# Kernel optimization log

Hardware: AMD Instinct MI355X
Metric: run time of the kernel (lower is better)

The kernel has to match this reference:

```python
import jax, jax.numpy as jnp
import numpy as np

THRESHOLD = 0.5
NEG_POS_RATIO = 3
ALPHA = 1.0
BETA = 1.0
IGNORE_INDEX = 255

B, P, C, O = 16, 16384, 21, 16
H = W = 256


def cxcy_to_xy(c):
    return jnp.concatenate([c[..., :2] - c[..., 2:] / 2, c[..., :2] + c[..., 2:] / 2], axis=-1)


def xy_to_cxcy(xy):
    return jnp.concatenate([(xy[..., :2] + xy[..., 2:]) / 2, xy[..., 2:] - xy[..., :2]], axis=-1)


def cxcy_to_gcxgcy(cxcy, priors_cxcy):
    return jnp.concatenate([
        (cxcy[..., :2] - priors_cxcy[..., :2]) / (priors_cxcy[..., 2:] / 10.0),
        jnp.log(cxcy[..., 2:] / priors_cxcy[..., 2:]) * 5.0,
    ], axis=-1)


def jaccard(set1, set2):
    # set1 [O,4] xy, set2 [P,4] xy -> IoU [O,P]
    lo = jnp.maximum(set1[:, None, :2], set2[None, :, :2])
    hi = jnp.minimum(set1[:, None, 2:], set2[None, :, 2:])
    wh = jnp.clip(hi - lo, 0.0)
    inter = wh[..., 0] * wh[..., 1]
    a1 = (set1[:, 2] - set1[:, 0]) * (set1[:, 3] - set1[:, 1])
    a2 = (set2[:, 2] - set2[:, 0]) * (set2[:, 3] - set2[:, 1])
    return inter / (a1[:, None] + a2[None, :] - inter)


def setup_inputs() -> dict:
    key = jax.random.key(0)
    ks = jax.random.split(key, 8)
    predicted_locs = jax.random.normal(ks[0], (B, P, 4), dtype=jnp.float32)
    predicted_scores = jax.random.normal(ks[1], (B, P, C), dtype=jnp.float32)
    predicted_masks = jax.random.normal(ks[2], (B, C, H, W), dtype=jnp.float32)
    x1y1 = jax.random.uniform(ks[3], (B, O, 2), dtype=jnp.float32) * 0.8
    wh = jax.random.uniform(ks[4], (B, O, 2), dtype=jnp.float32) * 0.19 + 0.01
    boxes = jnp.concatenate([x1y1, x1y1 + wh], axis=-1)  # valid xy boxes
    pc = jax.random.uniform(ks[5], (P, 2), dtype=jnp.float32) * 0.9 + 0.05
    pwh = jax.random.uniform(ks[6], (P, 2), dtype=jnp.float32) * 0.28 + 0.02
    priors_cxcy = jnp.concatenate([pc, pwh], axis=-1)
    labels = jax.random.randint(ks[7], (B, O), 1, C)  # object labels, never background
    masks = jax.random.randint(jax.random.fold_in(key, 99), (B, 1, H, W), 0, C)
    return {
        'predicted_locs': predicted_locs,
        'predicted_scores': predicted_scores,
        'predicted_masks': predicted_masks,
        'boxes': boxes,
        'priors_cxcy': priors_cxcy,
        'labels': labels,
        'masks': masks,
    }


def _assign(bx, lb, priors_cxcy, priors_xy):
    # bx [O,4] xy, lb [O] int -> true_locs [P,4], true_classes [P]
    ov = jaccard(bx, priors_xy)  # [O,P]
    overlap_for_each_prior = ov.max(axis=0)       # [P]
    object_for_each_prior = ov.argmax(axis=0)     # [P]
    prior_for_each_object = ov.argmax(axis=1)     # [O]
    # guarantee every object is matched to its best prior
    object_for_each_prior = object_for_each_prior.at[prior_for_each_object].set(jnp.arange(O))
    overlap_for_each_prior = overlap_for_each_prior.at[prior_for_each_object].set(1.0)
    label_for_each_prior = lb[object_for_each_prior]
    label_for_each_prior = jnp.where(overlap_for_each_prior < THRESHOLD, 0, label_for_each_prior)
    true_locs = cxcy_to_gcxgcy(xy_to_cxcy(bx[object_for_each_prior]), priors_cxcy)
    return true_locs, label_for_each_prior


def reference(predicted_locs, predicted_scores, predicted_masks, boxes, priors_cxcy, labels, masks):
    priors_xy = cxcy_to_xy(priors_cxcy)
    true_locs, true_classes = jax.vmap(_assign, in_axes=(0, 0, None, None))(
        boxes, labels, priors_cxcy, priors_xy)  # [B,P,4], [B,P]

    pos = true_classes != 0                      # [B,P]
    pos_f = pos.astype(predicted_locs.dtype)
    n_pos = pos.sum(axis=1)                      # [B]

    # localization: L1Loss (mean over positive prior elements)
    diff = jnp.abs(predicted_locs - true_locs)
    loc_loss = (diff * pos_f[..., None]).sum() / jnp.maximum(pos_f.sum() * 4.0, 1.0)

    # confidence: CE per prior + hard negative mining
    logp = jax.nn.log_softmax(predicted_scores, axis=-1)            # [B,P,C]
    ce = -jnp.take_along_axis(logp, true_classes[..., None], axis=-1)[..., 0]  # [B,P]
    ce_pos_sum = (ce * pos_f).sum()
    ce_neg = jnp.where(pos, 0.0, ce)
    ce_neg_sorted = -jnp.sort(-ce_neg, axis=1)                      # descending
    ranks = jnp.arange(P)[None, :]
    hard = (ranks < (NEG_POS_RATIO * n_pos)[:, None]).astype(ce.dtype)
    ce_hardneg_sum = (ce_neg_sorted * hard).sum()
    conf_loss = (ce_hardneg_sum + ce_pos_sum) / n_pos.sum().astype(ce.dtype)

    # mask loss: cross_entropy2d, sum reduction then / (H*W) / B
    tgt = masks[:, 0]                                                # [B,H,W]
    valid = (tgt != IGNORE_INDEX)
    t = jnp.where(valid, tgt, 0)
    logp_m = jax.nn.log_softmax(predicted_masks, axis=1)             # [B,C,H,W]
    ce_m = -jnp.take_along_axis(logp_m, t[:, None], axis=1)[:, 0]    # [B,H,W]
    mask_loss = (ce_m * valid.astype(ce_m.dtype)).sum() / (H * W) / B

    return conf_loss + ALPHA * loc_loss + BETA * mask_loss
```

## Files before the change

kernel.cpp:

```cpp
#include <hip/hip_runtime.h>
#include <cstdint>
#include <cstddef>

#define Bn 16
#define Pn 16384
#define Cn 21
#define On 16
#define HWn 65536
#define THRESH 0.5f


__device__ __forceinline__ float waveReduceSum(float v) {
  for (int off = 32; off > 0; off >>= 1) v += __shfl_down(v, off, 64);
  return v;
}
__device__ __forceinline__ int waveReduceSumI(int v) {
  for (int off = 32; off > 0; off >>= 1) v += __shfl_down(v, off, 64);
  return v;
}

__global__ __launch_bounds__(256, 2) void k_p1mask(
    const float* __restrict__ boxes, const float* __restrict__ priors,
    const float* __restrict__ pm, const int* __restrict__ msk,
    unsigned long long* __restrict__ partials, float* __restrict__ accum) {
  const int lane = threadIdx.x & 63, wave = threadIdx.x >> 6;
  __shared__ float4 sbox[On];
  __shared__ float sarea[On];
  __shared__ unsigned long long skey[On];
  __shared__ float sr1[4];

  if (blockIdx.x >= 1024) {
    const int idx4 = (blockIdx.x - 1024) * 256 + threadIdx.x;
    const int b = idx4 >> 14;
    const int pix = (idx4 & 16383) << 2;
    int4 t4 = ((const int4*)msk)[idx4];
    const float* base = pm + (size_t)b * ((size_t)Cn * HWn) + pix;
#define M_LD(i) float4 v##i = *(const float4*)(base + (size_t)(i) * HWn);
    M_LD(0) M_LD(1) M_LD(2) M_LD(3) M_LD(4) M_LD(5) M_LD(6) M_LD(7) M_LD(8)
    M_LD(9) M_LD(10) M_LD(11) M_LD(12) M_LD(13) M_LD(14) M_LD(15) M_LD(16)
    M_LD(17) M_LD(18) M_LD(19) M_LD(20)
#undef M_LD
    asm volatile("" ::"v"(v0.x), "v"(v1.x), "v"(v2.x), "v"(v3.x), "v"(v4.x),
                 "v"(v5.x), "v"(v6.x), "v"(v7.x), "v"(v8.x), "v"(v9.x),
                 "v"(v10.x), "v"(v11.x), "v"(v12.x), "v"(v13.x), "v"(v14.x),
                 "v"(v15.x), "v"(v16.x), "v"(v17.x), "v"(v18.x), "v"(v19.x),
                 "v"(v20.x));
    __builtin_amdgcn_sched_barrier(0);
    const bool q0 = (t4.x != 255), q1 = (t4.y != 255), q2 = (t4.z != 255),
               q3 = (t4.w != 255);
    const int c0 = q0 ? t4.x : 0, c1 = q1 ? t4.y : 0, c2 = q2 ? t4.z : 0,
              c3 = q3 ? t4.w : 0;
    float s0 = 0.f, s1 = 0.f, s2 = 0.f, s3 = 0.f;
    float x0 = 0.f, x1 = 0.f, x2 = 0.f, x3 = 0.f;
#define M_ACC(i)                                                            \
  {                                                                         \
    s0 += __expf(v##i.x); s1 += __expf(v##i.y);                             \
    s2 += __expf(v##i.z); s3 += __expf(v##i.w);                             \
    if (c0 == i) x0 = v##i.x; if (c1 == i) x1 = v##i.y;                     \
    if (c2 == i) x2 = v##i.z; if (c3 == i) x3 = v##i.w;                     \
  }
    M_ACC(0) M_ACC(1) M_ACC(2) M_ACC(3) M_ACC(4) M_ACC(5) M_ACC(6) M_ACC(7)
    M_ACC(8) M_ACC(9) M_ACC(10) M_ACC(11) M_ACC(12) M_ACC(13) M_ACC(14)
    M_ACC(15) M_ACC(16) M_ACC(17) M_ACC(18) M_ACC(19) M_ACC(20)
#undef M_ACC
    float contrib = (q0 ? (__logf(s0) - x0) : 0.f) +
                    (q1 ? (__logf(s1) - x1) : 0.f) +
                    (q2 ? (__logf(s2) - x2) : 0.f) +
                    (q3 ? (__logf(s3) - x3) : 0.f);
    float r = waveReduceSum(contrib);
    if (lane == 0) sr1[wave] = r;
    __syncthreads();
    if (threadIdx.x == 0)
      atomicAdd(&accum[3], sr1[0] + sr1[1] + sr1[2] + sr1[3]);
    return;
  }

  const int b = blockIdx.x >> 6;
  const int p0 = (blockIdx.x & 63) << 8;
  const int p = p0 + threadIdx.x;
  if (threadIdx.x < On) {
    float4 bx = ((const float4*)boxes)[b * On + threadIdx.x];
    sbox[threadIdx.x] = bx;
    sarea[threadIdx.x] = (bx.z - bx.x) * (bx.w - bx.y);
    skey[threadIdx.x] = 0ULL;
  }
  __syncthreads();
  float4 pr = ((const float4*)priors)[p];
  const float px1 = pr.x - 0.5f * pr.z, py1 = pr.y - 0.5f * pr.w;
  const float px2 = pr.x + 0.5f * pr.z, py2 = pr.y + 0.5f * pr.w;
  const float parea = pr.z * pr.w;
#pragma unroll
  for (int o = 0; o < On; ++o) {
    float4 bx = sbox[o];
    float ix = fmaxf(fminf(px2, bx.z) - fmaxf(px1, bx.x), 0.f);
    float iy = fmaxf(fminf(py2, bx.w) - fmaxf(py1, bx.y), 0.f);
    float inter = ix * iy;
    float iou = inter / (sarea[o] + parea - inter);
    float m = iou;
#pragma unroll
    for (int off = 32; off > 0; off >>= 1) m = fmaxf(m, __shfl_xor(m, off, 64));
    unsigned long long tie = __ballot(iou == m);
    if (lane == 0) {
      int lmin = __ffsll(tie) - 1;
      unsigned minp = (unsigned)(p0 + (wave << 6) + lmin);
      unsigned long long key = ((unsigned long long)__float_as_uint(m) << 32) |
                               (unsigned long long)(0xFFFFFFFFu - minp);
      atomicMax(&skey[o], key);
    }
  }
  __syncthreads();
  if (threadIdx.x < On)
    partials[(size_t)blockIdx.x * On + threadIdx.x] = skey[threadIdx.x];
}

__global__ __launch_bounds__(256, 2) void k_assign(
    const float* __restrict__ plocs, const float* __restrict__ pscores,
    const float* __restrict__ boxes, const float* __restrict__ priors,
    const int* __restrict__ labels, const unsigned long long* __restrict__ partials,
    float* __restrict__ ce_neg, float* __restrict__ accum,
    int* __restrict__ n_pos, int* __restrict__ n_pos_total) {
  __shared__ float ssc[256 * Cn];
  __shared__ float4 sbox[On];
  __shared__ float sarea[On];
  __shared__ int slab[On];
  __shared__ int spfo[On];
  __shared__ unsigned long long skey[On];
  __shared__ float sr1[4], sr2[4];
  __shared__ int sri[4];
  const int lane = threadIdx.x & 63, wave = threadIdx.x >> 6;
  const int b = blockIdx.x >> 6;
  const int p0 = (blockIdx.x & 63) << 8;
  const int p = p0 + threadIdx.x;
  {
    const float4* src = (const float4*)(pscores + ((size_t)b * Pn + p0) * Cn);
    float4* dst = (float4*)ssc;
#pragma unroll
    for (int i = threadIdx.x; i < (256 * Cn) / 4; i += 256) dst[i] = src[i];
  }
  if (threadIdx.x < On) skey[threadIdx.x] = 0ULL;
  if (threadIdx.x < On) {
    float4 bx = ((const float4*)boxes)[b * On + threadIdx.x];
    sbox[threadIdx.x] = bx;
    sarea[threadIdx.x] = (bx.z - bx.x) * (bx.w - bx.y);
    slab[threadIdx.x] = labels[b * On + threadIdx.x];
  }
  __syncthreads();
  {
    const int o = threadIdx.x & 15, j = threadIdx.x >> 4;
    const unsigned long long* pp = partials + ((size_t)b * 64) * On;
    unsigned long long k = 0ULL;
#pragma unroll
    for (int t = 0; t < 4; ++t) {
      unsigned long long v = pp[(size_t)(j * 4 + t) * On + o];
      k = v > k ? v : k;
    }
    atomicMax(&skey[o], k);
  }
  __syncthreads();
  if (threadIdx.x < On)
    spfo[threadIdx.x] = (int)(0xFFFFFFFFu - (unsigned)(skey[threadIdx.x] & 0xFFFFFFFFULL));
  __syncthreads();

  float4 pr = ((const float4*)priors)[p];
  const float px1 = pr.x - 0.5f * pr.z, py1 = pr.y - 0.5f * pr.w;
  const float px2 = pr.x + 0.5f * pr.z, py2 = pr.y + 0.5f * pr.w;
  const float parea = pr.z * pr.w;
  float best = -1.f;
  int bobj = 0;
#pragma unroll
  for (int o = 0; o < On; ++o) {
    float4 bx = sbox[o];
    float ix = fmaxf(fminf(px2, bx.z) - fmaxf(px1, bx.x), 0.f);
    float iy = fmaxf(fminf(py2, bx.w) - fmaxf(py1, bx.y), 0.f);
    float inter = ix * iy;
    float iou = inter / (sarea[o] + parea - inter);
    if (iou > best) { best = iou; bobj = o; }
  }
#pragma unroll
  for (int o = 0; o < On; ++o) {
    if (spfo[o] == p) { bobj = o; best = 1.0f; }
  }
  const int lbl = (best < THRESH) ? 0 : slab[bobj];
  const bool pos = (lbl != 0);
  float locp = 0.f;
  if (pos) {
    float4 bx = sbox[bobj];
    float cx = 0.5f * (bx.x + bx.z), cy = 0.5f * (bx.y + bx.w);
    float w = bx.z - bx.x, h = bx.w - bx.y;
    float g0 = (cx - pr.x) / (pr.z * 0.1f);
    float g1 = (cy - pr.y) / (pr.w * 0.1f);
    float g2 = logf(w / pr.z) * 5.f;
    float g3 = logf(h / pr.w) * 5.f;
    float4 pl = ((const float4*)plocs)[b * Pn + p];
    locp = fabsf(pl.x - g0) + fabsf(pl.y - g1) + fabsf(pl.z - g2) + fabsf(pl.w - g3);
  }
  const float* my = ssc + threadIdx.x * Cn;
  float s = 0.f, xt = 0.f;
#pragma unroll
  for (int c = 0; c < Cn; ++c) {
    float v = my[c];
    s += __expf(v);
    if (c == lbl) xt = v;
  }
  float ce = __logf(s) - xt;
  ce_neg[b * Pn + p] = pos ? 0.f : ce;
  float cep = pos ? ce : 0.f;

  float r1 = waveReduceSum(locp);
  float r2 = waveReduceSum(cep);
  int ri = waveReduceSumI(pos ? 1 : 0);
  if (lane == 0) { sr1[wave] = r1; sr2[wave] = r2; sri[wave] = ri; }
  __syncthreads();
  if (threadIdx.x == 0) {
    atomicAdd(&accum[0], sr1[0] + sr1[1] + sr1[2] + sr1[3]);
    atomicAdd(&accum[1], sr2[0] + sr2[1] + sr2[2] + sr2[3]);
    int ai = sri[0] + sri[1] + sri[2] + sri[3];
    atomicAdd(&n_pos[b], ai);
    atomicAdd(n_pos_total, ai);
  }
}

__global__ __launch_bounds__(1024) void k_hardneg_final(
    const float* __restrict__ ce_neg, const int* __restrict__ n_pos,
    float* __restrict__ accum, const int* __restrict__ n_pos_total,
    int* __restrict__ done_cnt, float* __restrict__ out) {
  const int b = blockIdx.x;
  const int lane = threadIdx.x & 63, wave = threadIdx.x >> 6;
  unsigned rv[16];
#pragma unroll
  for (int i = 0; i < 16; ++i)
    rv[i] = __float_as_uint(ce_neg[b * Pn + i * 1024 + threadIdx.x]);
  int K = 3 * n_pos[b];
  if (K > Pn) K = Pn;
  __shared__ int scnt[16];
  __shared__ float ssum[16];
  unsigned lo = 0u, hi = 0x7F800000u;
  while (lo < hi) {
    unsigned mid = lo + ((hi - lo) >> 1);
    int c = 0;
#pragma unroll
    for (int i = 0; i < 16; ++i) c += (rv[i] > mid) ? 1 : 0;
    c = waveReduceSumI(c);
    if (lane == 0) scnt[wave] = c;
    __syncthreads();
    int total = 0;
#pragma unroll
    for (int w = 0; w < 16; ++w) total += scnt[w];
    if (total < K) hi = mid; else lo = mid + 1;
    __syncthreads();
  }
  const float fv = __uint_as_float(lo);
  float s = 0.f;
  int c = 0;
#pragma unroll
  for (int i = 0; i < 16; ++i) {
    if (rv[i] > lo) { s += __uint_as_float(rv[i]); c++; }
  }
  s = waveReduceSum(s);
  c = waveReduceSumI(c);
  if (lane == 0) { ssum[wave] = s; scnt[wave] = c; }
  __syncthreads();
  if (threadIdx.x == 0) {
    float tots = 0.f;
    int totc = 0;
#pragma unroll
    for (int w = 0; w < 16; ++w) { tots += ssum[w]; totc += scnt[w]; }
    atomicAdd(&accum[2], tots + (float)(K - totc) * fv);
    __threadfence();
    int prev = atomicAdd(done_cnt, 1);
    if (prev == Bn - 1) {
      float a0 = atomicAdd(&accum[0], 0.f);
      float a1 = atomicAdd(&accum[1], 0.f);
      float a2 = atomicAdd(&accum[2], 0.f);
      float a3 = atomicAdd(&accum[3], 0.f);
      float np = (float)(*n_pos_total);
      float conf = (a2 + a1) / np;
      float loc = a0 / fmaxf(np * 4.f, 1.f);
      float maskl = a3 / (float)HWn / (float)Bn;
      out[0] = conf + loc + maskl;
    }
  }
}

extern "C" void kernel_launch(void* const* d_in, const int* in_sizes, int n_in,
                              void* d_out, int out_size, void* d_ws, size_t ws_size,
                              hipStream_t stream) {
  const float* plocs   = (const float*)d_in[0];
  const float* pscores = (const float*)d_in[1];
  const float* pmasks  = (const float*)d_in[2];
  const float* boxes   = (const float*)d_in[3];
  const float* priors  = (const float*)d_in[4];
  const int*   labels  = (const int*)d_in[5];
  const int*   masks   = (const int*)d_in[6];

  char* ws = (char*)d_ws;
  float* accum = (float*)ws;
  int* n_pos = (int*)(ws + 64);
  int* n_pos_total = (int*)(ws + 128);
  int* done_cnt = (int*)(ws + 132);
  unsigned long long* partials = (unsigned long long*)(ws + 4096);
  float* ce_neg = (float*)(ws + 135168);

  (void)hipMemsetAsync(ws, 0, 144, stream);
  k_p1mask<<<2048, 256, 0, stream>>>(boxes, priors, pmasks, masks, partials, accum);
  k_assign<<<1024, 256, 0, stream>>>(plocs, pscores, boxes, priors, labels,
                                     partials, ce_neg, accum, n_pos, n_pos_total);
  k_hardneg_final<<<Bn, 1024, 0, stream>>>(ce_neg, n_pos, accum, n_pos_total,
                                           done_cnt, (float*)d_out);
}
```

Before: 227.2 us.

## Fuse all stages into one cooperative persistent kernel with grid syncs

```diff
diff --git a/kernel.cpp b/kernel.cpp
--- a/kernel.cpp
+++ b/kernel.cpp
@@ -1,6 +1,9 @@
 #include <hip/hip_runtime.h>
+#include <hip/hip_cooperative_groups.h>
 #include <cstdint>
 #include <cstddef>
+
+namespace cg = cooperative_groups;
 
 #define Bn 16
 #define Pn 16384
@@ -19,18 +22,67 @@
   return v;
 }
 
-__global__ __launch_bounds__(256, 2) void k_p1mask(
-    const float* __restrict__ boxes, const float* __restrict__ priors,
-    const float* __restrict__ pm, const int* __restrict__ msk,
-    unsigned long long* __restrict__ partials, float* __restrict__ accum) {
-  const int lane = threadIdx.x & 63, wave = threadIdx.x >> 6;
+__global__ __launch_bounds__(256, 3) void k_all(
+    const float* __restrict__ plocs, const float* __restrict__ pscores,
+    const float* __restrict__ pm, const float* __restrict__ boxes,
+    const float* __restrict__ priors, const int* __restrict__ labels,
+    const int* __restrict__ msk, unsigned long long* __restrict__ partials,
+    float* __restrict__ ce_neg, float* __restrict__ mpart,
+    float* __restrict__ apart_loc, float* __restrict__ apart_ce,
+    int* __restrict__ apart_npos, float* __restrict__ bres,
+    float* __restrict__ out) {
+  __shared__ float ssc[256 * Cn];
   __shared__ float4 sbox[On];
   __shared__ float sarea[On];
+  __shared__ int slab[On];
+  __shared__ int spfo[On];
   __shared__ unsigned long long skey[On];
-  __shared__ float sr1[4];
-
-  if (blockIdx.x >= 1024) {
-    const int idx4 = (blockIdx.x - 1024) * 256 + threadIdx.x;
+  __shared__ float sr1[4], sr2[4];
+  __shared__ int sri[4];
+  const int tid = threadIdx.x;
+  const int lane = tid & 63, wave = tid >> 6;
+  cg::grid_group grid = cg::this_grid();
+
+  for (int t = blockIdx.x; t < Bn * 64; t += gridDim.x) {
+    const int b = t >> 6;
+    const int p0 = (t & 63) << 8;
+    const int p = p0 + tid;
+    if (tid < On) {
+      float4 bx = ((const float4*)boxes)[b * On + tid];
+      sbox[tid] = bx;
+      sarea[tid] = (bx.z - bx.x) * (bx.w - bx.y);
+      skey[tid] = 0ULL;
+    }
+    __syncthreads();
+    float4 pr = ((const float4*)priors)[p];
+    const float px1 = pr.x - 0.5f * pr.z, py1 = pr.y - 0.5f * pr.w;
+    const float px2 = pr.x + 0.5f * pr.z, py2 = pr.y + 0.5f * pr.w;
+    const float parea = pr.z * pr.w;
+#pragma unroll
+    for (int o = 0; o < On; ++o) {
+      float4 bx = sbox[o];
+      float ix = fmaxf(fminf(px2, bx.z) - fmaxf(px1, bx.x), 0.f);
+      float iy = fmaxf(fminf(py2, bx.w) - fmaxf(py1, bx.y), 0.f);
+      float inter = ix * iy;
+      float iou = inter / (sarea[o] + parea - inter);
+      float m = iou;
+#pragma unroll
+      for (int off = 32; off > 0; off >>= 1) m = fmaxf(m, __shfl_xor(m, off, 64));
+      unsigned long long tie = __ballot(iou == m);
+      if (lane == 0) {
+        int lmin = __ffsll(tie) - 1;
+        unsigned minp = (unsigned)(p0 + (wave << 6) + lmin);
+        unsigned long long key = ((unsigned long long)__float_as_uint(m) << 32) |
+                                 (unsigned long long)(0xFFFFFFFFu - minp);
+        atomicMax(&skey[o], key);
+      }
+    }
+    __syncthreads();
+    if (tid < On) partials[(size_t)t * On + tid] = skey[tid];
+  }
+
+  for (int t = blockIdx.x; t < 1024; t += gridDim.x) {
+    const int idx4 = t * 256 + tid;
     const int b = idx4 >> 14;
     const int pix = (idx4 & 16383) << 2;
     int4 t4 = ((const int4*)msk)[idx4];
@@ -70,210 +122,185 @@
     float r = waveReduceSum(contrib);
     if (lane == 0) sr1[wave] = r;
     __syncthreads();
-    if (threadIdx.x == 0)
-      atomicAdd(&accum[3], sr1[0] + sr1[1] + sr1[2] + sr1[3]);
-    return;
-  }
-
-  const int b = blockIdx.x >> 6;
-  const int p0 = (blockIdx.x & 63) << 8;
-  const int p = p0 + threadIdx.x;
-  if (threadIdx.x < On) {
-    float4 bx = ((const float4*)boxes)[b * On + threadIdx.x];
-    sbox[threadIdx.x] = bx;
-    sarea[threadIdx.x] = (bx.z - bx.x) * (bx.w - bx.y);
-    skey[threadIdx.x] = 0ULL;
-  }
-  __syncthreads();
-  float4 pr = ((const float4*)priors)[p];
-  const float px1 = pr.x - 0.5f * pr.z, py1 = pr.y - 0.5f * pr.w;
-  const float px2 = pr.x + 0.5f * pr.z, py2 = pr.y + 0.5f * pr.w;
-  const float parea = pr.z * pr.w;
-#pragma unroll
-  for (int o = 0; o < On; ++o) {
-    float4 bx = sbox[o];
-    float ix = fmaxf(fminf(px2, bx.z) - fmaxf(px1, bx.x), 0.f);
-    float iy = fmaxf(fminf(py2, bx.w) - fmaxf(py1, bx.y), 0.f);
-    float inter = ix * iy;
-    float iou = inter / (sarea[o] + parea - inter);
-    float m = iou;
-#pragma unroll
-    for (int off = 32; off > 0; off >>= 1) m = fmaxf(m, __shfl_xor(m, off, 64));
-    unsigned long long tie = __ballot(iou == m);
+    if (tid == 0) mpart[t] = sr1[0] + sr1[1] + sr1[2] + sr1[3];
+    __syncthreads();
+  }
+
+  __threadfence();
+  grid.sync();
+
+  for (int t = blockIdx.x; t < Bn * 64; t += gridDim.x) {
+    const int b = t >> 6;
+    const int p0 = (t & 63) << 8;
+    const int p = p0 + tid;
+    {
+      const float4* src = (const float4*)(pscores + ((size_t)b * Pn + p0) * Cn);
+      float4* dst = (float4*)ssc;
+#pragma unroll
+      for (int i = tid; i < (256 * Cn) / 4; i += 256) dst[i] = src[i];
+    }
+    if (tid < On) {
+      float4 bx = ((const float4*)boxes)[b * On + tid];
+      sbox[tid] = bx;
+      sarea[tid] = (bx.z - bx.x) * (bx.w - bx.y);
+      slab[tid] = labels[b * On + tid];
+      skey[tid] = 0ULL;
+    }
+    __syncthreads();
+    {
+      const int o = tid & 15, j = tid >> 4;
+      const unsigned long long* pp = partials + ((size_t)b * 64) * On;
+      unsigned long long k = 0ULL;
+#pragma unroll
+      for (int q = 0; q < 4; ++q) {
+        unsigned long long v = pp[(size_t)(j * 4 + q) * On + o];
+        k = v > k ? v : k;
+      }
+      atomicMax(&skey[o], k);
+    }
+    __syncthreads();
+    if (tid < On)
+      spfo[tid] = (int)(0xFFFFFFFFu - (unsigned)(skey[tid] & 0xFFFFFFFFULL));
+    __syncthreads();
+
+    float4 pr = ((const float4*)priors)[p];
+    const float px1 = pr.x - 0.5f * pr.z, py1 = pr.y - 0.5f * pr.w;
+    const float px2 = pr.x + 0.5f * pr.z, py2 = pr.y + 0.5f * pr.w;
+    const float parea = pr.z * pr.w;
+    float best = -1.f;
+    int bobj = 0;
+#pragma unroll
+    for (int o = 0; o < On; ++o) {
+      float4 bx = sbox[o];
+      float ix = fmaxf(fminf(px2, bx.z) - fmaxf(px1, bx.x), 0.f);
+      float iy = fmaxf(fminf(py2, bx.w) - fmaxf(py1, bx.y), 0.f);
+      float inter = ix * iy;
+      float iou = inter / (sarea[o] + parea - inter);
+      if (iou > best) { best = iou; bobj = o; }
+    }
+#pragma unroll
+    for (int o = 0; o < On; ++o) {
+      if (spfo[o] == p) { bobj = o; best = 1.0f; }
+    }
+    const int lbl = (best < THRESH) ? 0 : slab[bobj];
+    const bool pos = (lbl != 0);
+    float locp = 0.f;
+    if (pos) {
+      float4 bx = sbox[bobj];
+      float cx = 0.5f * (bx.x + bx.z), cy = 0.5f * (bx.y + bx.w);
+      float w = bx.z - bx.x, h = bx.w - bx.y;
+      float g0 = (cx - pr.x) / (pr.z * 0.1f);
+      float g1 = (cy - pr.y) / (pr.w * 0.1f);
+      float g2 = logf(w / pr.z) * 5.f;
+      float g3 = logf(h / pr.w) * 5.f;
+      float4 pl = ((const float4*)plocs)[b * Pn + p];
+      locp = fabsf(pl.x - g0) + fabsf(pl.y - g1) + fabsf(pl.z - g2) +
+             fabsf(pl.w - g3);
+    }
+    const float* my = ssc + tid * Cn;
+    float s = 0.f, xt = 0.f;
+#pragma unroll
+    for (int c = 0; c < Cn; ++c) {
+      float v = my[c];
+      s += __expf(v);
+      if (c == lbl) xt = v;
+    }
+    float ce = __logf(s) - xt;
+    ce_neg[b * Pn + p] = pos ? 0.f : ce;
+    float cep = pos ? ce : 0.f;
+
+    float r1 = waveReduceSum(locp);
+    float r2 = waveReduceSum(cep);
+    int ri = waveReduceSumI(pos ? 1 : 0);
+    if (lane == 0) { sr1[wave] = r1; sr2[wave] = r2; sri[wave] = ri; }
+    __syncthreads();
+    if (tid == 0) {
+      apart_loc[t] = sr1[0] + sr1[1] + sr1[2] + sr1[3];
+      apart_ce[t] = sr2[0] + sr2[1] + sr2[2] + sr2[3];
+      apart_npos[t] = sri[0] + sri[1] + sri[2] + sri[3];
+    }
+  }
+
+  __threadfence();
+  grid.sync();
+
+  if (blockIdx.x < Bn) {
+    const int b = blockIdx.x;
+    unsigned rv[64];
+#pragma unroll
+    for (int i = 0; i < 64; ++i)
+      rv[i] = __float_as_uint(ce_neg[b * Pn + i * 256 + tid]);
+    if (wave == 0) {
+      int v = apart_npos[b * 64 + lane];
+      v = waveReduceSumI(v);
+      if (lane == 0) spfo[0] = v;
+    }
+    __syncthreads();
+    int K = 3 * spfo[0];
+    if (K > Pn) K = Pn;
+    unsigned lo = 0u, hi = 0x7F800000u;
+    while (lo < hi) {
+      unsigned mid = lo + ((hi - lo) >> 1);
+      int c = 0;
+#pragma unroll
+      for (int i = 0; i < 64; ++i) c += (rv[i] > mid) ? 1 : 0;
+      c = waveReduceSumI(c);
+      if (lane == 0) sri[wave] = c;
+      __syncthreads();
+      int total = sri[0] + sri[1] + sri[2] + sri[3];
+      if (total < K) hi = mid; else lo = mid + 1;
+      __syncthreads();
+    }
+    const float fv = __uint_as_float(lo);
+    float s = 0.f;
+    int c = 0;
+#pragma unroll
+    for (int i = 0; i < 64; ++i) {
+      if (rv[i] > lo) { s += __uint_as_float(rv[i]); c++; }
+    }
+    s = waveReduceSum(s);
+    c = waveReduceSumI(c);
+    if (lane == 0) { sr1[wave] = s; sri[wave] = c; }
+    __syncthreads();
+    if (tid == 0) {
+      float tots = sr1[0] + sr1[1] + sr1[2] + sr1[3];
+      int totc = sri[0] + sri[1] + sri[2] + sri[3];
+      bres[b] = tots + (float)(K - totc) * fv;
+    }
+  }
+
+  __threadfence();
+  grid.sync();
+
+  if (blockIdx.x == 0) {
+    float l_loc = 0.f, l_ce = 0.f, l_msk = 0.f;
+    int l_np = 0;
+    for (int i = tid; i < 1024; i += 256) {
+      l_loc += apart_loc[i];
+      l_ce += apart_ce[i];
+      l_msk += mpart[i];
+      l_np += apart_npos[i];
+    }
+    float l_hn = (tid < Bn) ? bres[tid] : 0.f;
+    l_loc = waveReduceSum(l_loc);
+    l_ce = waveReduceSum(l_ce);
+    l_msk = waveReduceSum(l_msk);
+    l_hn = waveReduceSum(l_hn);
+    int l_npw = waveReduceSumI(l_np);
     if (lane == 0) {
-      int lmin = __ffsll(tie) - 1;
-      unsigned minp = (unsigned)(p0 + (wave << 6) + lmin);
-      unsigned long long key = ((unsigned long long)__float_as_uint(m) << 32) |
-                               (unsigned long long)(0xFFFFFFFFu - minp);
-      atomicMax(&skey[o], key);
-    }
-  }
-  __syncthreads();
-  if (threadIdx.x < On)
-    partials[(size_t)blockIdx.x * On + threadIdx.x] = skey[threadIdx.x];
-}
-
-__global__ __launch_bounds__(256, 2) void k_assign(
-    const float* __restrict__ plocs, const float* __restrict__ pscores,
-    const float* __restrict__ boxes, const float* __restrict__ priors,
-    const int* __restrict__ labels, const unsigned long long* __restrict__ partials,
-    float* __restrict__ ce_neg, float* __restrict__ accum,
-    int* __restrict__ n_pos, int* __restrict__ n_pos_total) {
-  __shared__ float ssc[256 * Cn];
-  __shared__ float4 sbox[On];
-  __shared__ float sarea[On];
-  __shared__ int slab[On];
-  __shared__ int spfo[On];
-  __shared__ unsigned long long skey[On];
-  __shared__ float sr1[4], sr2[4];
-  __shared__ int sri[4];
-  const int lane = threadIdx.x & 63, wave = threadIdx.x >> 6;
-  const int b = blockIdx.x >> 6;
-  const int p0 = (blockIdx.x & 63) << 8;
-  const int p = p0 + threadIdx.x;
-  {
-    const float4* src = (const float4*)(pscores + ((size_t)b * Pn + p0) * Cn);
-    float4* dst = (float4*)ssc;
-#pragma unroll
-    for (int i = threadIdx.x; i < (256 * Cn) / 4; i += 256) dst[i] = src[i];
-  }
-  if (threadIdx.x < On) skey[threadIdx.x] = 0ULL;
-  if (threadIdx.x < On) {
-    float4 bx = ((const float4*)boxes)[b * On + threadIdx.x];
-    sbox[threadIdx.x] = bx;
-    sarea[threadIdx.x] = (bx.z - bx.x) * (bx.w - bx.y);
-    slab[threadIdx.x] = labels[b * On + threadIdx.x];
-  }
-  __syncthreads();
-  {
-    const int o = threadIdx.x & 15, j = threadIdx.x >> 4;
-    const unsigned long long* pp = partials + ((size_t)b * 64) * On;
-    unsigned long long k = 0ULL;
-#pragma unroll
-    for (int t = 0; t < 4; ++t) {
-      unsigned long long v = pp[(size_t)(j * 4 + t) * On + o];
-      k = v > k ? v : k;
-    }
-    atomicMax(&skey[o], k);
-  }
-  __syncthreads();
-  if (threadIdx.x < On)
-    spfo[threadIdx.x] = (int)(0xFFFFFFFFu - (unsigned)(skey[threadIdx.x] & 0xFFFFFFFFULL));
-  __syncthreads();
-
-  float4 pr = ((const float4*)priors)[p];
-  const float px1 = pr.x - 0.5f * pr.z, py1 = pr.y - 0.5f * pr.w;
-  const float px2 = pr.x + 0.5f * pr.z, py2 = pr.y + 0.5f * pr.w;
-  const float parea = pr.z * pr.w;
-  float best = -1.f;
-  int bobj = 0;
-#pragma unroll
-  for (int o = 0; o < On; ++o) {
-    float4 bx = sbox[o];
-    float ix = fmaxf(fminf(px2, bx.z) - fmaxf(px1, bx.x), 0.f);
-    float iy = fmaxf(fminf(py2, bx.w) - fmaxf(py1, bx.y), 0.f);
-    float inter = ix * iy;
-    float iou = inter / (sarea[o] + parea - inter);
-    if (iou > best) { best = iou; bobj = o; }
-  }
-#pragma unroll
-  for (int o = 0; o < On; ++o) {
-    if (spfo[o] == p) { bobj = o; best = 1.0f; }
-  }
-  const int lbl = (best < THRESH) ? 0 : slab[bobj];
-  const bool pos = (lbl != 0);
-  float locp = 0.f;
-  if (pos) {
-    float4 bx = sbox[bobj];
-    float cx = 0.5f * (bx.x + bx.z), cy = 0.5f * (bx.y + bx.w);
-    float w = bx.z - bx.x, h = bx.w - bx.y;
-    float g0 = (cx - pr.x) / (pr.z * 0.1f);
-    float g1 = (cy - pr.y) / (pr.w * 0.1f);
-    float g2 = logf(w / pr.z) * 5.f;
-    float g3 = logf(h / pr.w) * 5.f;
-    float4 pl = ((const float4*)plocs)[b * Pn + p];
-    locp = fabsf(pl.x - g0) + fabsf(pl.y - g1) + fabsf(pl.z - g2) + fabsf(pl.w - g3);
-  }
-  const float* my = ssc + threadIdx.x * Cn;
-  float s = 0.f, xt = 0.f;
-#pragma unroll
-  for (int c = 0; c < Cn; ++c) {
-    float v = my[c];
-    s += __expf(v);
-    if (c == lbl) xt = v;
-  }
-  float ce = __logf(s) - xt;
-  ce_neg[b * Pn + p] = pos ? 0.f : ce;
-  float cep = pos ? ce : 0.f;
-
-  float r1 = waveReduceSum(locp);
-  float r2 = waveReduceSum(cep);
-  int ri = waveReduceSumI(pos ? 1 : 0);
-  if (lane == 0) { sr1[wave] = r1; sr2[wave] = r2; sri[wave] = ri; }
-  __syncthreads();
-  if (threadIdx.x == 0) {
-    atomicAdd(&accum[0], sr1[0] + sr1[1] + sr1[2] + sr1[3]);
-    atomicAdd(&accum[1], sr2[0] + sr2[1] + sr2[2] + sr2[3]);
-    int ai = sri[0] + sri[1] + sri[2] + sri[3];
-    atomicAdd(&n_pos[b], ai);
-    atomicAdd(n_pos_total, ai);
-  }
-}
-
-__global__ __launch_bounds__(1024) void k_hardneg_final(
-    const float* __restrict__ ce_neg, const int* __restrict__ n_pos,
-    float* __restrict__ accum, const int* __restrict__ n_pos_total,
-    int* __restrict__ done_cnt, float* __restrict__ out) {
-  const int b = blockIdx.x;
-  const int lane = threadIdx.x & 63, wave = threadIdx.x >> 6;
-  unsigned rv[16];
-#pragma unroll
-  for (int i = 0; i < 16; ++i)
-    rv[i] = __float_as_uint(ce_neg[b * Pn + i * 1024 + threadIdx.x]);
-  int K = 3 * n_pos[b];
-  if (K > Pn) K = Pn;
-  __shared__ int scnt[16];
-  __shared__ float ssum[16];
-  unsigned lo = 0u, hi = 0x7F800000u;
-  while (lo < hi) {
-    unsigned mid = lo + ((hi - lo) >> 1);
-    int c = 0;
-#pragma unroll
-    for (int i = 0; i < 16; ++i) c += (rv[i] > mid) ? 1 : 0;
-    c = waveReduceSumI(c);
-    if (lane == 0) scnt[wave] = c;
-    __syncthreads();
-    int total = 0;
-#pragma unroll
-    for (int w = 0; w < 16; ++w) total += scnt[w];
-    if (total < K) hi = mid; else lo = mid + 1;
-    __syncthreads();
-  }
-  const float fv = __uint_as_float(lo);
-  float s = 0.f;
-  int c = 0;
-#pragma unroll
-  for (int i = 0; i < 16; ++i) {
-    if (rv[i] > lo) { s += __uint_as_float(rv[i]); c++; }
-  }
-  s = waveReduceSum(s);
-  c = waveReduceSumI(c);
-  if (lane == 0) { ssum[wave] = s; scnt[wave] = c; }
-  __syncthreads();
-  if (threadIdx.x == 0) {
-    float tots = 0.f;
-    int totc = 0;
-#pragma unroll
-    for (int w = 0; w < 16; ++w) { tots += ssum[w]; totc += scnt[w]; }
-    atomicAdd(&accum[2], tots + (float)(K - totc) * fv);
-    __threadfence();
-    int prev = atomicAdd(done_cnt, 1);
-    if (prev == Bn - 1) {
-      float a0 = atomicAdd(&accum[0], 0.f);
-      float a1 = atomicAdd(&accum[1], 0.f);
-      float a2 = atomicAdd(&accum[2], 0.f);
-      float a3 = atomicAdd(&accum[3], 0.f);
-      float np = (float)(*n_pos_total);
+      ssc[wave] = l_loc;
+      ssc[4 + wave] = l_ce;
+      ssc[8 + wave] = l_msk;
+      ssc[12 + wave] = l_hn;
+      sri[wave] = l_npw;
+    }
+    __syncthreads();
+    if (tid == 0) {
+      float a0 = ssc[0] + ssc[1] + ssc[2] + ssc[3];
+      float a1 = ssc[4] + ssc[5] + ssc[6] + ssc[7];
+      float a3 = ssc[8] + ssc[9] + ssc[10] + ssc[11];
+      float a2 = ssc[12] + ssc[13] + ssc[14] + ssc[15];
+      float np = (float)(sri[0] + sri[1] + sri[2] + sri[3]);
       float conf = (a2 + a1) / np;
       float loc = a0 / fmaxf(np * 4.f, 1.f);
       float maskl = a3 / (float)HWn / (float)Bn;
@@ -294,17 +321,35 @@
   const int*   masks   = (const int*)d_in[6];
 
   char* ws = (char*)d_ws;
-  float* accum = (float*)ws;
-  int* n_pos = (int*)(ws + 64);
-  int* n_pos_total = (int*)(ws + 128);
-  int* done_cnt = (int*)(ws + 132);
+  float* mpart = (float*)ws;
   unsigned long long* partials = (unsigned long long*)(ws + 4096);
   float* ce_neg = (float*)(ws + 135168);
-
-  (void)hipMemsetAsync(ws, 0, 144, stream);
-  k_p1mask<<<2048, 256, 0, stream>>>(boxes, priors, pmasks, masks, partials, accum);
-  k_assign<<<1024, 256, 0, stream>>>(plocs, pscores, boxes, priors, labels,
-                                     partials, ce_neg, accum, n_pos, n_pos_total);
-  k_hardneg_final<<<Bn, 1024, 0, stream>>>(ce_neg, n_pos, accum, n_pos_total,
-                                           done_cnt, (float*)d_out);
+  float* apart_loc = (float*)(ws + 1183744);
+  float* apart_ce = (float*)(ws + 1187840);
+  int* apart_npos = (int*)(ws + 1191936);
+  float* bres = (float*)(ws + 1196032);
+  float* outf = (float*)d_out;
+
+  static int nblocks = 0;
+  if (nblocks == 0) {
+    int perCU = 0;
+    (void)hipOccupancyMaxActiveBlocksPerMultiprocessor(&perCU, k_all, 256, 0);
+    if (perCU < 1) perCU = 1;
+    int dev = 0;
+    (void)hipGetDevice(&dev);
+    hipDeviceProp_t prop;
+    (void)hipGetDeviceProperties(&prop, dev);
+    long total = (long)perCU * (long)prop.multiProcessorCount;
+    if (total > 1024) total = 1024;
+    if (total < Bn) total = Bn;
+    nblocks = (int)total;
+  }
+
+  void* args[] = {(void*)&plocs,   (void*)&pscores, (void*)&pmasks,
+                  (void*)&boxes,   (void*)&priors,  (void*)&labels,
+                  (void*)&masks,   (void*)&partials, (void*)&ce_neg,
+                  (void*)&mpart,   (void*)&apart_loc, (void*)&apart_ce,
+                  (void*)&apart_npos, (void*)&bres,  (void*)&outf};
+  (void)hipLaunchCooperativeKernel(k_all, dim3(nblocks), dim3(256), args, 0,
+                                   stream);
 }
```

New measurement: 487.8 us. 2.15x slower.

## Replace global atomics and memset with per-block partials and software-pipelined mask loads

Applied to the files above, without the earlier changes.

```diff
diff --git a/kernel.cpp b/kernel.cpp
--- a/kernel.cpp
+++ b/kernel.cpp
@@ -19,15 +19,18 @@
   return v;
 }
 
-__global__ __launch_bounds__(256, 2) void k_p1mask(
+__global__ __launch_bounds__(256) void k_p1mask(
     const float* __restrict__ boxes, const float* __restrict__ priors,
     const float* __restrict__ pm, const int* __restrict__ msk,
-    unsigned long long* __restrict__ partials, float* __restrict__ accum) {
+    unsigned long long* __restrict__ partials, float* __restrict__ mpart,
+    int* __restrict__ done_cnt) {
   const int lane = threadIdx.x & 63, wave = threadIdx.x >> 6;
   __shared__ float4 sbox[On];
   __shared__ float sarea[On];
   __shared__ unsigned long long skey[On];
   __shared__ float sr1[4];
+
+  if (blockIdx.x == 0 && threadIdx.x == 0) *done_cnt = 0;
 
   if (blockIdx.x >= 1024) {
     const int idx4 = (blockIdx.x - 1024) * 256 + threadIdx.x;
@@ -35,43 +38,41 @@
     const int pix = (idx4 & 16383) << 2;
     int4 t4 = ((const int4*)msk)[idx4];
     const float* base = pm + (size_t)b * ((size_t)Cn * HWn) + pix;
-#define M_LD(i) float4 v##i = *(const float4*)(base + (size_t)(i) * HWn);
-    M_LD(0) M_LD(1) M_LD(2) M_LD(3) M_LD(4) M_LD(5) M_LD(6) M_LD(7) M_LD(8)
-    M_LD(9) M_LD(10) M_LD(11) M_LD(12) M_LD(13) M_LD(14) M_LD(15) M_LD(16)
-    M_LD(17) M_LD(18) M_LD(19) M_LD(20)
-#undef M_LD
-    asm volatile("" ::"v"(v0.x), "v"(v1.x), "v"(v2.x), "v"(v3.x), "v"(v4.x),
-                 "v"(v5.x), "v"(v6.x), "v"(v7.x), "v"(v8.x), "v"(v9.x),
-                 "v"(v10.x), "v"(v11.x), "v"(v12.x), "v"(v13.x), "v"(v14.x),
-                 "v"(v15.x), "v"(v16.x), "v"(v17.x), "v"(v18.x), "v"(v19.x),
-                 "v"(v20.x));
-    __builtin_amdgcn_sched_barrier(0);
-    const bool q0 = (t4.x != 255), q1 = (t4.y != 255), q2 = (t4.z != 255),
-               q3 = (t4.w != 255);
-    const int c0 = q0 ? t4.x : 0, c1 = q1 ? t4.y : 0, c2 = q2 ? t4.z : 0,
-              c3 = q3 ? t4.w : 0;
+#define M_LD(i) (*(const float4*)(base + (size_t)(i) * HWn))
+    float4 q0 = M_LD(0), q1 = M_LD(1), q2 = M_LD(2), q3 = M_LD(3);
+    float4 q4 = M_LD(4), q5 = M_LD(5), q6 = M_LD(6), q7 = M_LD(7);
+    const bool w0 = (t4.x != 255), w1 = (t4.y != 255), w2 = (t4.z != 255),
+               w3 = (t4.w != 255);
+    const int c0 = w0 ? t4.x : 0, c1 = w1 ? t4.y : 0, c2 = w2 ? t4.z : 0,
+              c3 = w3 ? t4.w : 0;
     float s0 = 0.f, s1 = 0.f, s2 = 0.f, s3 = 0.f;
     float x0 = 0.f, x1 = 0.f, x2 = 0.f, x3 = 0.f;
-#define M_ACC(i)                                                            \
+#define M_ACC(v, c)                                                         \
   {                                                                         \
-    s0 += __expf(v##i.x); s1 += __expf(v##i.y);                             \
-    s2 += __expf(v##i.z); s3 += __expf(v##i.w);                             \
-    if (c0 == i) x0 = v##i.x; if (c1 == i) x1 = v##i.y;                     \
-    if (c2 == i) x2 = v##i.z; if (c3 == i) x3 = v##i.w;                     \
-  }
-    M_ACC(0) M_ACC(1) M_ACC(2) M_ACC(3) M_ACC(4) M_ACC(5) M_ACC(6) M_ACC(7)
-    M_ACC(8) M_ACC(9) M_ACC(10) M_ACC(11) M_ACC(12) M_ACC(13) M_ACC(14)
-    M_ACC(15) M_ACC(16) M_ACC(17) M_ACC(18) M_ACC(19) M_ACC(20)
+    s0 += __expf(v.x); s1 += __expf(v.y);                                   \
+    s2 += __expf(v.z); s3 += __expf(v.w);                                   \
+    if (c0 == c) x0 = v.x; if (c1 == c) x1 = v.y;                           \
+    if (c2 == c) x2 = v.z; if (c3 == c) x3 = v.w;                           \
+  }
+#define M_STEP(r, c, pf) { float4 t = r; r = M_LD(pf); M_ACC(t, c) }
+    M_STEP(q0, 0, 8)  M_STEP(q1, 1, 9)  M_STEP(q2, 2, 10) M_STEP(q3, 3, 11)
+    M_STEP(q4, 4, 12) M_STEP(q5, 5, 13) M_STEP(q6, 6, 14) M_STEP(q7, 7, 15)
+    M_STEP(q0, 8, 16) M_STEP(q1, 9, 17) M_STEP(q2, 10, 18) M_STEP(q3, 11, 19)
+    M_STEP(q4, 12, 20)
+    M_ACC(q5, 13) M_ACC(q6, 14) M_ACC(q7, 15) M_ACC(q0, 16)
+    M_ACC(q1, 17) M_ACC(q2, 18) M_ACC(q3, 19) M_ACC(q4, 20)
+#undef M_STEP
 #undef M_ACC
-    float contrib = (q0 ? (__logf(s0) - x0) : 0.f) +
-                    (q1 ? (__logf(s1) - x1) : 0.f) +
-                    (q2 ? (__logf(s2) - x2) : 0.f) +
-                    (q3 ? (__logf(s3) - x3) : 0.f);
+#undef M_LD
+    float contrib = (w0 ? (__logf(s0) - x0) : 0.f) +
+                    (w1 ? (__logf(s1) - x1) : 0.f) +
+                    (w2 ? (__logf(s2) - x2) : 0.f) +
+                    (w3 ? (__logf(s3) - x3) : 0.f);
     float r = waveReduceSum(contrib);
     if (lane == 0) sr1[wave] = r;
     __syncthreads();
     if (threadIdx.x == 0)
-      atomicAdd(&accum[3], sr1[0] + sr1[1] + sr1[2] + sr1[3]);
+      mpart[blockIdx.x - 1024] = sr1[0] + sr1[1] + sr1[2] + sr1[3];
     return;
   }
 
@@ -117,8 +118,8 @@
     const float* __restrict__ plocs, const float* __restrict__ pscores,
     const float* __restrict__ boxes, const float* __restrict__ priors,
     const int* __restrict__ labels, const unsigned long long* __restrict__ partials,
-    float* __restrict__ ce_neg, float* __restrict__ accum,
-    int* __restrict__ n_pos, int* __restrict__ n_pos_total) {
+    float* __restrict__ ce_neg, float* __restrict__ apart_loc,
+    float* __restrict__ apart_ce, int* __restrict__ apart_npos) {
   __shared__ float ssc[256 * Cn];
   __shared__ float4 sbox[On];
   __shared__ float sarea[On];
@@ -137,12 +138,12 @@
 #pragma unroll
     for (int i = threadIdx.x; i < (256 * Cn) / 4; i += 256) dst[i] = src[i];
   }
-  if (threadIdx.x < On) skey[threadIdx.x] = 0ULL;
   if (threadIdx.x < On) {
     float4 bx = ((const float4*)boxes)[b * On + threadIdx.x];
     sbox[threadIdx.x] = bx;
     sarea[threadIdx.x] = (bx.z - bx.x) * (bx.w - bx.y);
     slab[threadIdx.x] = labels[b * On + threadIdx.x];
+    skey[threadIdx.x] = 0ULL;
   }
   __syncthreads();
   {
@@ -212,28 +213,35 @@
   if (lane == 0) { sr1[wave] = r1; sr2[wave] = r2; sri[wave] = ri; }
   __syncthreads();
   if (threadIdx.x == 0) {
-    atomicAdd(&accum[0], sr1[0] + sr1[1] + sr1[2] + sr1[3]);
-    atomicAdd(&accum[1], sr2[0] + sr2[1] + sr2[2] + sr2[3]);
-    int ai = sri[0] + sri[1] + sri[2] + sri[3];
-    atomicAdd(&n_pos[b], ai);
-    atomicAdd(n_pos_total, ai);
+    apart_loc[blockIdx.x] = sr1[0] + sr1[1] + sr1[2] + sr1[3];
+    apart_ce[blockIdx.x] = sr2[0] + sr2[1] + sr2[2] + sr2[3];
+    apart_npos[blockIdx.x] = sri[0] + sri[1] + sri[2] + sri[3];
   }
 }
 
 __global__ __launch_bounds__(1024) void k_hardneg_final(
-    const float* __restrict__ ce_neg, const int* __restrict__ n_pos,
-    float* __restrict__ accum, const int* __restrict__ n_pos_total,
+    const float* __restrict__ ce_neg, const int* __restrict__ apart_npos,
+    const float* __restrict__ apart_loc, const float* __restrict__ apart_ce,
+    const float* __restrict__ mpart, float* __restrict__ bres,
     int* __restrict__ done_cnt, float* __restrict__ out) {
   const int b = blockIdx.x;
-  const int lane = threadIdx.x & 63, wave = threadIdx.x >> 6;
-  unsigned rv[16];
-#pragma unroll
-  for (int i = 0; i < 16; ++i)
-    rv[i] = __float_as_uint(ce_neg[b * Pn + i * 1024 + threadIdx.x]);
-  int K = 3 * n_pos[b];
-  if (K > Pn) K = Pn;
+  const int tid = threadIdx.x;
+  const int lane = tid & 63, wave = tid >> 6;
   __shared__ int scnt[16];
   __shared__ float ssum[16];
+  __shared__ int sK;
+  unsigned rv[16];
+#pragma unroll
+  for (int i = 0; i < 16; ++i)
+    rv[i] = __float_as_uint(ce_neg[b * Pn + i * 1024 + tid]);
+  if (wave == 0) {
+    int v = (lane < 64) ? apart_npos[b * 64 + lane] : 0;
+    v = waveReduceSumI(v);
+    if (lane == 0) sK = v;
+  }
+  __syncthreads();
+  int K = 3 * sK;
+  if (K > Pn) K = Pn;
   unsigned lo = 0u, hi = 0x7F800000u;
   while (lo < hi) {
     unsigned mid = lo + ((hi - lo) >> 1);
@@ -260,25 +268,53 @@
   c = waveReduceSumI(c);
   if (lane == 0) { ssum[wave] = s; scnt[wave] = c; }
   __syncthreads();
-  if (threadIdx.x == 0) {
+  if (tid == 0) {
     float tots = 0.f;
     int totc = 0;
 #pragma unroll
     for (int w = 0; w < 16; ++w) { tots += ssum[w]; totc += scnt[w]; }
-    atomicAdd(&accum[2], tots + (float)(K - totc) * fv);
+    bres[b] = tots + (float)(K - totc) * fv;
+  }
+  __syncthreads();
+
+  if (tid == 0) {
     __threadfence();
-    int prev = atomicAdd(done_cnt, 1);
-    if (prev == Bn - 1) {
-      float a0 = atomicAdd(&accum[0], 0.f);
-      float a1 = atomicAdd(&accum[1], 0.f);
-      float a2 = atomicAdd(&accum[2], 0.f);
-      float a3 = atomicAdd(&accum[3], 0.f);
-      float np = (float)(*n_pos_total);
-      float conf = (a2 + a1) / np;
-      float loc = a0 / fmaxf(np * 4.f, 1.f);
-      float maskl = a3 / (float)HWn / (float)Bn;
-      out[0] = conf + loc + maskl;
+    scnt[0] = atomicAdd(done_cnt, 1);
+  }
+  __syncthreads();
+  if (scnt[0] != Bn - 1) return;
+  __threadfence();
+  float l_loc = apart_loc[tid];
+  float l_ce = apart_ce[tid];
+  float l_msk = mpart[tid];
+  int l_np = apart_npos[tid];
+  float l_hn = (tid < Bn) ? atomicAdd(&bres[tid], 0.f) : 0.f;
+  l_loc = waveReduceSum(l_loc);
+  l_ce = waveReduceSum(l_ce);
+  l_msk = waveReduceSum(l_msk);
+  l_hn = waveReduceSum(l_hn);
+  int l_npw = waveReduceSumI(l_np);
+  if (lane == 0) {
+    ssum[wave] = l_loc;
+    scnt[wave] = l_npw;
+  }
+  __syncthreads();
+  __shared__ float sce[16], smk[16], shn[16];
+  if (lane == 0) { sce[wave] = l_ce; smk[wave] = l_msk; shn[wave] = l_hn; }
+  __syncthreads();
+  if (tid == 0) {
+    float a0 = 0.f, a1 = 0.f, a2 = 0.f, a3 = 0.f;
+    int np_i = 0;
+#pragma unroll
+    for (int w = 0; w < 16; ++w) {
+      a0 += ssum[w]; a1 += sce[w]; a3 += smk[w]; a2 += shn[w];
+      np_i += scnt[w];
     }
+    float np = (float)np_i;
+    float conf = (a2 + a1) / np;
+    float loc = a0 / fmaxf(np * 4.f, 1.f);
+    float maskl = a3 / (float)HWn / (float)Bn;
+    out[0] = conf + loc + maskl;
   }
 }
 
@@ -294,17 +330,21 @@
   const int*   masks   = (const int*)d_in[6];
 
   char* ws = (char*)d_ws;
-  float* accum = (float*)ws;
-  int* n_pos = (int*)(ws + 64);
-  int* n_pos_total = (int*)(ws + 128);
-  int* done_cnt = (int*)(ws + 132);
+  float* mpart = (float*)ws;
   unsigned long long* partials = (unsigned long long*)(ws + 4096);
   float* ce_neg = (float*)(ws + 135168);
-
-  (void)hipMemsetAsync(ws, 0, 144, stream);
-  k_p1mask<<<2048, 256, 0, stream>>>(boxes, priors, pmasks, masks, partials, accum);
+  float* apart_loc = (float*)(ws + 1183744);
+  float* apart_ce = (float*)(ws + 1187840);
+  int* apart_npos = (int*)(ws + 1191936);
+  float* bres = (float*)(ws + 1196032);
+  int* done_cnt = (int*)(ws + 1196160);
+
+  k_p1mask<<<2048, 256, 0, stream>>>(boxes, priors, pmasks, masks, partials,
+                                     mpart, done_cnt);
   k_assign<<<1024, 256, 0, stream>>>(plocs, pscores, boxes, priors, labels,
-                                     partials, ce_neg, accum, n_pos, n_pos_total);
-  k_hardneg_final<<<Bn, 1024, 0, stream>>>(ce_neg, n_pos, accum, n_pos_total,
-                                           done_cnt, (float*)d_out);
-}
+                                     partials, ce_neg, apart_loc, apart_ce,
+                                     apart_npos);
+  k_hardneg_final<<<Bn, 1024, 0, stream>>>(ce_neg, apart_npos, apart_loc,
+                                           apart_ce, mpart, bres, done_cnt,
+                                           (float*)d_out);
+}
```

Result: faster. 201.0 us (-11.5%).
